# Kernel tuning notes

Hardware: AMD Instinct MI355X
Metric: run time of the kernel (lower is better)

Reference implementation:

```python
import jax, jax.numpy as jnp
import numpy as np
from jax import lax

BN_EPS = 1e-5

def _dw_conv_bn(img, w, g, b, mu, var):
    # img: [B,C,H,W], w: [C,1,3,3] depthwise (feature_group_count=C), stride 1, pad 1
    C = img.shape[1]
    y = lax.conv_general_dilated(img, w, (1, 1), 'SAME',
                                 dimension_numbers=('NCHW', 'OIHW', 'NCHW'),
                                 feature_group_count=C)
    scale = (g / jnp.sqrt(var + BN_EPS))[None, :, None, None]
    return y * scale + (b - mu * g / jnp.sqrt(var + BN_EPS))[None, :, None, None]


def setup_inputs() -> dict:
    key = jax.random.key(0)
    B, H, W, C, Co = 32, 28, 28, 192, 192
    T = 1 + H * W
    ks = jax.random.split(key, 8)
    x = jax.random.normal(ks[0], (B, T, C), dtype=jnp.float32)
    conv_w = jax.random.normal(ks[1], (3, C, 1, 3, 3), dtype=jnp.float32) * 0.1
    bn_scale = 1.0 + 0.1 * jax.random.normal(ks[2], (3, C), dtype=jnp.float32)
    bn_bias = 0.1 * jax.random.normal(ks[3], (3, C), dtype=jnp.float32)
    bn_mean = 0.1 * jax.random.normal(ks[4], (3, C), dtype=jnp.float32)
    bn_var = jax.random.uniform(ks[5], (3, C), dtype=jnp.float32, minval=0.5, maxval=1.5)
    w_qkv = jax.random.normal(ks[6], (3, Co, C), dtype=jnp.float32) / np.sqrt(C)
    kp, kb = jax.random.split(ks[7])
    w_proj = jax.random.normal(kp, (Co, Co), dtype=jnp.float32) / np.sqrt(Co)
    b_proj = 0.01 * jax.random.normal(kb, (Co,), dtype=jnp.float32)
    return {"x": x, "conv_w": conv_w, "bn_scale": bn_scale, "bn_bias": bn_bias,
            "bn_mean": bn_mean, "bn_var": bn_var, "w_qkv": w_qkv,
            "w_proj": w_proj, "b_proj": b_proj, "h": H, "w": W, "num_heads": 3}


def reference(x, conv_w, bn_scale, bn_bias, bn_mean, bn_var, w_qkv, w_proj, b_proj, h, w, num_heads):
    B, T, C = x.shape
    Co = w_proj.shape[0]
    scale = Co ** (-0.5)  # NOTE: module scales by dim_out^-0.5, not per-head
    cls_tok, tok = x[:, :1], x[:, 1:]
    img = tok.reshape(B, h, w, C).transpose(0, 3, 1, 2)  # b (h w) c -> b c h w
    qkv = []
    for i in range(3):  # q, k, v conv projections (depthwise conv + BN inference)
        y = _dw_conv_bn(img, conv_w[i], bn_scale[i], bn_bias[i], bn_mean[i], bn_var[i])
        y = y.reshape(B, C, h * w).transpose(0, 2, 1)  # b c h w -> b (h w) c
        y = jnp.concatenate([cls_tok, y], axis=1)      # prepend cls token
        qkv.append(jnp.einsum('btc,oc->bto', y, w_qkv[i]))
    d = Co // num_heads
    q, k, v = (t.reshape(B, T, num_heads, d).transpose(0, 2, 1, 3) for t in qkv)
    attn = jnp.einsum('bhld,bhtd->bhlt', q, k) * scale
    attn = jax.nn.softmax(attn, axis=-1)
    out = jnp.einsum('bhlt,bhtd->bhld', attn, v)
    out = out.transpose(0, 2, 1, 3).reshape(B, T, Co)
    return out @ w_proj.T + b_proj
```

## Files before the change

kernel.cpp:

```cpp
#include <hip/hip_runtime.h>

#define B_   32
#define Hh   28
#define Ww   28
#define Cc   192
#define T_   785
#define BT_  (B_ * T_)
#define BTC_ ((size_t)BT_ * Cc)
#define SCALE 0.07216878364870323f

typedef __attribute__((ext_vector_type(8))) __bf16 bf16x8;
typedef __attribute__((ext_vector_type(4))) __bf16 bf16x4;
typedef __attribute__((ext_vector_type(4))) float  f32x4;

__device__ __forceinline__ int imin(int a, int b) { return a < b ? a : b; }

__global__ void wcvt_k(const float* __restrict__ src, __bf16* __restrict__ dst, int n) {
  int i = blockIdx.x * 256 + threadIdx.x;
  if (i < n) dst[i] = (__bf16)src[i];
}

__global__ __launch_bounds__(192) void conv3_bn_k(
    const float* __restrict__ x, const float* __restrict__ cw,
    const float* __restrict__ g, const float* __restrict__ bb,
    const float* __restrict__ mu, const float* __restrict__ var,
    __bf16* __restrict__ y)
{
  const int c = threadIdx.x;
  const int h = blockIdx.x;
  const int b = blockIdx.y;
  float w9[3][9], sc[3], sh[3];
#pragma unroll
  for (int br = 0; br < 3; ++br) {
    sc[br] = g[br * Cc + c] * rsqrtf(var[br * Cc + c] + 1e-5f);
    sh[br] = bb[br * Cc + c] - mu[br * Cc + c] * sc[br];
#pragma unroll
    for (int k = 0; k < 9; ++k) w9[br][k] = cw[(br * Cc + c) * 9 + k];
  }
  const float* xb = x + (size_t)b * T_ * Cc;
  if (h == 0) {
#pragma unroll
    for (int br = 0; br < 3; ++br)
      y[br * BTC_ + (size_t)b * T_ * Cc + c] = (__bf16)xb[c];
  }
  float c0[3], c1[3], c2[3];
#pragma unroll
  for (int r = 0; r < 3; ++r) {
    int rr = h - 1 + r;
    c0[r] = 0.f;
    c1[r] = (rr >= 0 && rr < Hh) ? xb[(size_t)(1 + rr * Ww) * Cc + c] : 0.f;
  }
  for (int col = 0; col < Ww; ++col) {
#pragma unroll
    for (int r = 0; r < 3; ++r) {
      int rr = h - 1 + r, ci = col + 1;
      c2[r] = (rr >= 0 && rr < Hh && ci < Ww)
                ? xb[(size_t)(1 + rr * Ww + ci) * Cc + c] : 0.f;
    }
    size_t orow = (size_t)(b * T_ + 1 + h * Ww + col) * Cc + c;
#pragma unroll
    for (int br = 0; br < 3; ++br) {
      float acc = c0[0]*w9[br][0] + c1[0]*w9[br][1] + c2[0]*w9[br][2]
                + c0[1]*w9[br][3] + c1[1]*w9[br][4] + c2[1]*w9[br][5]
                + c0[2]*w9[br][6] + c1[2]*w9[br][7] + c2[2]*w9[br][8];
      y[br * BTC_ + orow] = (__bf16)(acc * sc[br] + sh[br]);
    }
#pragma unroll
    for (int r = 0; r < 3; ++r) { c0[r] = c1[r]; c1[r] = c2[r]; }
  }
}

template <int OUTF32>
__global__ __launch_bounds__(256) void gemm_bf16(
    const __bf16* __restrict__ A, const __bf16* __restrict__ Bw,
    const float* __restrict__ bias, void* __restrict__ outp, float oscale)
{
  __shared__ __bf16 As[128][72];
  __shared__ __bf16 Bs[64][72];
  const int tid = threadIdx.x;
  const int wid = tid >> 6, l = tid & 63, c = l & 15, g = l >> 4;
  const int wm = wid >> 1, wn = wid & 1;
  const int m0 = blockIdx.x * 128, n0 = blockIdx.y * 64;
  const int ar = tid >> 1, ah = tid & 1;
  const int br2 = tid >> 2, bq = tid & 3;

  f32x4 acc[4][2];
#pragma unroll
  for (int i = 0; i < 4; ++i)
#pragma unroll
    for (int j = 0; j < 2; ++j) acc[i][j] = (f32x4)(0.f);

  for (int kc = 0; kc < 3; ++kc) {
    const int k0 = kc * 64;
    const __bf16* ap = A + (size_t)imin(m0 + ar, BT_ - 1) * Cc + k0 + ah * 32;
    const __bf16* bp = Bw + (size_t)(n0 + br2) * Cc + k0 + bq * 16;
    uint4 a0 = *(const uint4*)(ap + 0);
    uint4 a1 = *(const uint4*)(ap + 8);
    uint4 a2 = *(const uint4*)(ap + 16);
    uint4 a3 = *(const uint4*)(ap + 24);
    uint4 b0 = *(const uint4*)(bp + 0);
    uint4 b1 = *(const uint4*)(bp + 8);
    __syncthreads();
    *(uint4*)&As[ar][ah * 32 + 0]  = a0;
    *(uint4*)&As[ar][ah * 32 + 8]  = a1;
    *(uint4*)&As[ar][ah * 32 + 16] = a2;
    *(uint4*)&As[ar][ah * 32 + 24] = a3;
    *(uint4*)&Bs[br2][bq * 16 + 0] = b0;
    *(uint4*)&Bs[br2][bq * 16 + 8] = b1;
    __syncthreads();
#pragma unroll
    for (int ksl = 0; ksl < 2; ++ksl) {
      bf16x8 af[4], bfr[2];
#pragma unroll
      for (int mf = 0; mf < 4; ++mf)
        af[mf] = *(const bf16x8*)&As[wm * 64 + mf * 16 + c][ksl * 32 + g * 8];
#pragma unroll
      for (int nf = 0; nf < 2; ++nf)
        bfr[nf] = *(const bf16x8*)&Bs[wn * 32 + nf * 16 + c][ksl * 32 + g * 8];
#pragma unroll
      for (int mf = 0; mf < 4; ++mf)
#pragma unroll
        for (int nf = 0; nf < 2; ++nf)
          acc[mf][nf] = __builtin_amdgcn_mfma_f32_16x16x32_bf16(
              af[mf], bfr[nf], acc[mf][nf], 0, 0, 0);
    }
  }
  float bias_c[2] = {0.f, 0.f};
  if (OUTF32) {
#pragma unroll
    for (int nf = 0; nf < 2; ++nf) bias_c[nf] = bias[n0 + wn * 32 + nf * 16 + c];
  }
#pragma unroll
  for (int mf = 0; mf < 4; ++mf) {
#pragma unroll
    for (int i = 0; i < 4; ++i) {
      int m = m0 + wm * 64 + mf * 16 + g * 4 + i;
      if (m < BT_) {
#pragma unroll
        for (int nf = 0; nf < 2; ++nf) {
          int n = n0 + wn * 32 + nf * 16 + c;
          if (OUTF32)
            ((float*)outp)[(size_t)m * Cc + n] = acc[mf][nf][i] + bias_c[nf];
          else
            ((__bf16*)outp)[(size_t)m * Cc + n] = (__bf16)(acc[mf][nf][i] * oscale);
        }
      }
    }
  }
}

__global__ __launch_bounds__(256) void attn_mfma(
    const __bf16* __restrict__ qkv, __bf16* __restrict__ aout)
{
  __shared__ __bf16 Ks[64][72];
  __shared__ __bf16 Vt[64][72];
  __shared__ __bf16 Ps[4][16][72];
  const int tid = threadIdx.x;
  const int wid = tid >> 6, l = tid & 63, c = l & 15, g = l >> 4;
  const int qt = blockIdx.x, hh = blockIdx.y, b = blockIdx.z;
  const __bf16* Q = qkv + ((size_t)(0 * B_ + b) * T_) * Cc + hh * 64;
  const __bf16* K = qkv + ((size_t)(1 * B_ + b) * T_) * Cc + hh * 64;
  const __bf16* V = qkv + ((size_t)(2 * B_ + b) * T_) * Cc + hh * 64;

  const int qrow = qt * 64 + wid * 16 + c;
  const __bf16* qp = Q + (size_t)imin(qrow, T_ - 1) * Cc + g * 8;
  bf16x8 qf[2];
  qf[0] = *(const bf16x8*)(qp);
  qf[1] = *(const bf16x8*)(qp + 32);

  const int skey = tid >> 2, sdq = tid & 3;
  const int vkp = tid & 31, vd0 = (tid >> 5) * 8;

  f32x4 ot[4];
#pragma unroll
  for (int f = 0; f < 4; ++f) ot[f] = (f32x4)(0.f);
  float m_run = -1e30f, l_run = 0.f;

  for (int kt = 0; kt < 13; ++kt) {
    __syncthreads();
    {
      const __bf16* kp = K + (size_t)imin(kt * 64 + skey, T_ - 1) * Cc + sdq * 16;
      uint4 k0v = *(const uint4*)(kp + 0);
      uint4 k1v = *(const uint4*)(kp + 8);
      *(uint4*)&Ks[skey][sdq * 16 + 0] = k0v;
      *(uint4*)&Ks[skey][sdq * 16 + 8] = k1v;
      const __bf16* v0 = V + (size_t)imin(kt * 64 + 2 * vkp + 0, T_ - 1) * Cc + vd0;
      const __bf16* v1 = V + (size_t)imin(kt * 64 + 2 * vkp + 1, T_ - 1) * Cc + vd0;
      uint4 va = *(const uint4*)v0;
      uint4 vb = *(const uint4*)v1;
      const ushort* pa = (const ushort*)&va;
      const ushort* pb = (const ushort*)&vb;
#pragma unroll
      for (int e = 0; e < 8; ++e) {
        unsigned pk = (unsigned)pa[e] | ((unsigned)pb[e] << 16);
        *(unsigned*)&Vt[vd0 + e][2 * vkp] = pk;
      }
    }
    __syncthreads();

    f32x4 st[4];
#pragma unroll
    for (int f = 0; f < 4; ++f) st[f] = (f32x4)(0.f);
#pragma unroll
    for (int s = 0; s < 2; ++s) {
#pragma unroll
      for (int f = 0; f < 4; ++f) {
        bf16x8 ka = *(const bf16x8*)&Ks[f * 16 + c][s * 32 + g * 8];
        st[f] = __builtin_amdgcn_mfma_f32_16x16x32_bf16(ka, qf[s], st[f], 0, 0, 0);
      }
    }
    if (kt == 12) {
#pragma unroll
      for (int f = 0; f < 4; ++f)
#pragma unroll
        for (int i = 0; i < 4; ++i)
          if (f * 16 + g * 4 + i >= 17) st[f][i] = -1e30f;
    }
    float pmax = -1e30f;
#pragma unroll
    for (int f = 0; f < 4; ++f)
#pragma unroll
      for (int i = 0; i < 4; ++i) pmax = fmaxf(pmax, st[f][i]);
    pmax = fmaxf(pmax, __shfl_xor(pmax, 16));
    pmax = fmaxf(pmax, __shfl_xor(pmax, 32));
    float mnew = fmaxf(m_run, pmax);
    float corr = __expf(m_run - mnew);
    m_run = mnew;
    float rs = 0.f;
#pragma unroll
    for (int f = 0; f < 4; ++f) {
      bf16x4 pk;
#pragma unroll
      for (int i = 0; i < 4; ++i) {
        float p = __expf(st[f][i] - mnew);
        rs += p;
        pk[i] = (__bf16)p;
      }
      *(bf16x4*)&Ps[wid][c][f * 16 + g * 4] = pk;
    }
    rs += __shfl_xor(rs, 16);
    rs += __shfl_xor(rs, 32);
    l_run = l_run * corr + rs;
#pragma unroll
    for (int f = 0; f < 4; ++f)
#pragma unroll
      for (int i = 0; i < 4; ++i) ot[f][i] *= corr;

#pragma unroll
    for (int s = 0; s < 2; ++s) {
      bf16x8 pb2 = *(const bf16x8*)&Ps[wid][c][s * 32 + g * 8];
#pragma unroll
      for (int f = 0; f < 4; ++f) {
        bf16x8 va2 = *(const bf16x8*)&Vt[f * 16 + c][s * 32 + g * 8];
        ot[f] = __builtin_amdgcn_mfma_f32_16x16x32_bf16(va2, pb2, ot[f], 0, 0, 0);
      }
    }
  }

  const int t = qt * 64 + wid * 16 + c;
  if (t < T_) {
    float inv = l_run > 0.f ? 1.f / l_run : 0.f;
    __bf16* op = aout + ((size_t)(b * T_ + t)) * Cc + hh * 64;
#pragma unroll
    for (int f = 0; f < 4; ++f) {
      bf16x4 ov;
#pragma unroll
      for (int i = 0; i < 4; ++i) ov[i] = (__bf16)(ot[f][i] * inv);
      *(bf16x4*)(op + f * 16 + g * 4) = ov;
    }
  }
}

extern "C" void kernel_launch(void* const* d_in, const int* in_sizes, int n_in,
                              void* d_out, int out_size, void* d_ws, size_t ws_size,
                              hipStream_t stream) {
  (void)in_sizes; (void)n_in; (void)out_size; (void)ws_size;
  const float* x        = (const float*)d_in[0];
  const float* conv_w   = (const float*)d_in[1];
  const float* bn_scale = (const float*)d_in[2];
  const float* bn_bias  = (const float*)d_in[3];
  const float* bn_mean  = (const float*)d_in[4];
  const float* bn_var   = (const float*)d_in[5];
  const float* w_qkv    = (const float*)d_in[6];
  const float* w_proj   = (const float*)d_in[7];
  const float* b_proj   = (const float*)d_in[8];

  __bf16* ybf  = (__bf16*)d_ws;
  __bf16* qkvb = ybf + 3 * BTC_;
  __bf16* aobf = qkvb + 3 * BTC_;
  __bf16* wq   = aobf + BTC_;
  __bf16* wp   = wq + 3 * Cc * Cc;

  wcvt_k<<<(3 * Cc * Cc + 255) / 256, 256, 0, stream>>>(w_qkv, wq, 3 * Cc * Cc);
  wcvt_k<<<(Cc * Cc + 255) / 256, 256, 0, stream>>>(w_proj, wp, Cc * Cc);
  conv3_bn_k<<<dim3(Hh, B_), 192, 0, stream>>>(
      x, conv_w, bn_scale, bn_bias, bn_mean, bn_var, ybf);

  const int mblocks = (BT_ + 127) / 128;
  for (int i = 0; i < 3; ++i) {
    gemm_bf16<0><<<dim3(mblocks, 3), 256, 0, stream>>>(
        ybf + (size_t)i * BTC_, wq + (size_t)i * Cc * Cc, nullptr,
        qkvb + (size_t)i * BTC_, i == 0 ? SCALE : 1.0f);
  }
  attn_mfma<<<dim3(13, 3, B_), 256, 0, stream>>>(qkvb, aobf);
  gemm_bf16<1><<<dim3(mblocks, 3), 256, 0, stream>>>(
      aobf, wp, b_proj, d_out, 1.0f);
}
```

Baseline: 186.7 us.

## Batch launches, prefetch tiles, use exp2 softmax with lazy rescale, swizzle attention blocks

Merges the two weight-conversion launches and the three QKV GEMM launches into single launches, and makes the conv kernel produce two output rows per block to reuse loaded input rows. Both the GEMM and the attention kernel now register-prefetch the next K-chunk or K/V tile while the current one is stored to and computed from shared memory. The attention softmax folds log2(e) into the Q scale so it can use exp2f, and it rescales the running max and accumulator only when the new max exceeds the old one by more than a threshold. Attention blocks are also launched from a 1D swizzled index. These changes aim to cut launch overhead, hide global-load latency and reduce exp and rescale work, at the cost of more registers and a softmax whose unnormalised values may grow before the final divide.

```diff
diff --git a/kernel.cpp b/kernel.cpp
--- a/kernel.cpp
+++ b/kernel.cpp
@@ -7,7 +7,7 @@
 #define T_   785
 #define BT_  (B_ * T_)
 #define BTC_ ((size_t)BT_ * Cc)
-#define SCALE 0.07216878364870323f
+#define SCALE2 0.10412163388f
 
 typedef __attribute__((ext_vector_type(8))) __bf16 bf16x8;
 typedef __attribute__((ext_vector_type(4))) __bf16 bf16x4;
@@ -15,9 +15,11 @@
 
 __device__ __forceinline__ int imin(int a, int b) { return a < b ? a : b; }
 
-__global__ void wcvt_k(const float* __restrict__ src, __bf16* __restrict__ dst, int n) {
+__global__ void wcvt_k(const float* __restrict__ wq, const float* __restrict__ wp,
+                       __bf16* __restrict__ dst) {
   int i = blockIdx.x * 256 + threadIdx.x;
-  if (i < n) dst[i] = (__bf16)src[i];
+  float v = (i < 3 * Cc * Cc) ? wq[i] : wp[i - 3 * Cc * Cc];
+  dst[i] = (__bf16)v;
 }
 
 __global__ __launch_bounds__(192) void conv3_bn_k(
@@ -27,7 +29,7 @@
     __bf16* __restrict__ y)
 {
   const int c = threadIdx.x;
-  const int h = blockIdx.x;
+  const int h0 = blockIdx.x * 2;
   const int b = blockIdx.y;
   float w9[3][9], sc[3], sh[3];
 #pragma unroll
@@ -38,45 +40,52 @@
     for (int k = 0; k < 9; ++k) w9[br][k] = cw[(br * Cc + c) * 9 + k];
   }
   const float* xb = x + (size_t)b * T_ * Cc;
-  if (h == 0) {
+  if (h0 == 0) {
 #pragma unroll
     for (int br = 0; br < 3; ++br)
       y[br * BTC_ + (size_t)b * T_ * Cc + c] = (__bf16)xb[c];
   }
-  float c0[3], c1[3], c2[3];
-#pragma unroll
-  for (int r = 0; r < 3; ++r) {
-    int rr = h - 1 + r;
+  float c0[4], c1[4], c2[4];
+#pragma unroll
+  for (int r = 0; r < 4; ++r) {
+    int rr = h0 - 1 + r;
     c0[r] = 0.f;
     c1[r] = (rr >= 0 && rr < Hh) ? xb[(size_t)(1 + rr * Ww) * Cc + c] : 0.f;
   }
   for (int col = 0; col < Ww; ++col) {
 #pragma unroll
-    for (int r = 0; r < 3; ++r) {
-      int rr = h - 1 + r, ci = col + 1;
+    for (int r = 0; r < 4; ++r) {
+      int rr = h0 - 1 + r, ci = col + 1;
       c2[r] = (rr >= 0 && rr < Hh && ci < Ww)
                 ? xb[(size_t)(1 + rr * Ww + ci) * Cc + c] : 0.f;
     }
-    size_t orow = (size_t)(b * T_ + 1 + h * Ww + col) * Cc + c;
-#pragma unroll
-    for (int br = 0; br < 3; ++br) {
-      float acc = c0[0]*w9[br][0] + c1[0]*w9[br][1] + c2[0]*w9[br][2]
-                + c0[1]*w9[br][3] + c1[1]*w9[br][4] + c2[1]*w9[br][5]
-                + c0[2]*w9[br][6] + c1[2]*w9[br][7] + c2[2]*w9[br][8];
-      y[br * BTC_ + orow] = (__bf16)(acc * sc[br] + sh[br]);
-    }
-#pragma unroll
-    for (int r = 0; r < 3; ++r) { c0[r] = c1[r]; c1[r] = c2[r]; }
-  }
-}
-
-template <int OUTF32>
+#pragma unroll
+    for (int ro = 0; ro < 2; ++ro) {
+      size_t orow = (size_t)(b * T_ + 1 + (h0 + ro) * Ww + col) * Cc + c;
+#pragma unroll
+      for (int br = 0; br < 3; ++br) {
+        float acc = c0[ro+0]*w9[br][0] + c1[ro+0]*w9[br][1] + c2[ro+0]*w9[br][2]
+                  + c0[ro+1]*w9[br][3] + c1[ro+1]*w9[br][4] + c2[ro+1]*w9[br][5]
+                  + c0[ro+2]*w9[br][6] + c1[ro+2]*w9[br][7] + c2[ro+2]*w9[br][8];
+        y[br * BTC_ + orow] = (__bf16)(acc * sc[br] + sh[br]);
+      }
+    }
+#pragma unroll
+    for (int r = 0; r < 4; ++r) { c0[r] = c1[r]; c1[r] = c2[r]; }
+  }
+}
+
+template <int MODE>
 __global__ __launch_bounds__(256) void gemm_bf16(
-    const __bf16* __restrict__ A, const __bf16* __restrict__ Bw,
-    const float* __restrict__ bias, void* __restrict__ outp, float oscale)
+    const __bf16* __restrict__ A0, const __bf16* __restrict__ W0,
+    const float* __restrict__ bias, void* __restrict__ outp)
 {
   __shared__ __bf16 As[128][72];
   __shared__ __bf16 Bs[64][72];
+  const int z = blockIdx.z;
+  const __bf16* A  = A0 + (MODE == 0 ? (size_t)z * BTC_ : 0);
+  const __bf16* Bw = W0 + (MODE == 0 ? (size_t)z * Cc * Cc : 0);
+  const float oscale = (MODE == 0 && z == 0) ? SCALE2 : 1.0f;
   const int tid = threadIdx.x;
   const int wid = tid >> 6, l = tid & 63, c = l & 15, g = l >> 4;
   const int wm = wid >> 1, wn = wid & 1;
@@ -90,16 +99,16 @@
 #pragma unroll
     for (int j = 0; j < 2; ++j) acc[i][j] = (f32x4)(0.f);
 
+  const __bf16* ap = A + (size_t)imin(m0 + ar, BT_ - 1) * Cc + ah * 32;
+  const __bf16* bp = Bw + (size_t)(n0 + br2) * Cc + bq * 16;
+  uint4 a0 = *(const uint4*)(ap + 0);
+  uint4 a1 = *(const uint4*)(ap + 8);
+  uint4 a2 = *(const uint4*)(ap + 16);
+  uint4 a3 = *(const uint4*)(ap + 24);
+  uint4 b0 = *(const uint4*)(bp + 0);
+  uint4 b1 = *(const uint4*)(bp + 8);
+
   for (int kc = 0; kc < 3; ++kc) {
-    const int k0 = kc * 64;
-    const __bf16* ap = A + (size_t)imin(m0 + ar, BT_ - 1) * Cc + k0 + ah * 32;
-    const __bf16* bp = Bw + (size_t)(n0 + br2) * Cc + k0 + bq * 16;
-    uint4 a0 = *(const uint4*)(ap + 0);
-    uint4 a1 = *(const uint4*)(ap + 8);
-    uint4 a2 = *(const uint4*)(ap + 16);
-    uint4 a3 = *(const uint4*)(ap + 24);
-    uint4 b0 = *(const uint4*)(bp + 0);
-    uint4 b1 = *(const uint4*)(bp + 8);
     __syncthreads();
     *(uint4*)&As[ar][ah * 32 + 0]  = a0;
     *(uint4*)&As[ar][ah * 32 + 8]  = a1;
@@ -107,6 +116,15 @@
     *(uint4*)&As[ar][ah * 32 + 24] = a3;
     *(uint4*)&Bs[br2][bq * 16 + 0] = b0;
     *(uint4*)&Bs[br2][bq * 16 + 8] = b1;
+    if (kc < 2) {
+      ap += 64; bp += 64;
+      a0 = *(const uint4*)(ap + 0);
+      a1 = *(const uint4*)(ap + 8);
+      a2 = *(const uint4*)(ap + 16);
+      a3 = *(const uint4*)(ap + 24);
+      b0 = *(const uint4*)(bp + 0);
+      b1 = *(const uint4*)(bp + 8);
+    }
     __syncthreads();
 #pragma unroll
     for (int ksl = 0; ksl < 2; ++ksl) {
@@ -126,7 +144,7 @@
     }
   }
   float bias_c[2] = {0.f, 0.f};
-  if (OUTF32) {
+  if (MODE == 1) {
 #pragma unroll
     for (int nf = 0; nf < 2; ++nf) bias_c[nf] = bias[n0 + wn * 32 + nf * 16 + c];
   }
@@ -139,10 +157,11 @@
 #pragma unroll
         for (int nf = 0; nf < 2; ++nf) {
           int n = n0 + wn * 32 + nf * 16 + c;
-          if (OUTF32)
+          if (MODE == 1)
             ((float*)outp)[(size_t)m * Cc + n] = acc[mf][nf][i] + bias_c[nf];
           else
-            ((__bf16*)outp)[(size_t)m * Cc + n] = (__bf16)(acc[mf][nf][i] * oscale);
+            ((__bf16*)outp)[z * BTC_ + (size_t)m * Cc + n] =
+                (__bf16)(acc[mf][nf][i] * oscale);
         }
       }
     }
@@ -155,9 +174,14 @@
   __shared__ __bf16 Ks[64][72];
   __shared__ __bf16 Vt[64][72];
   __shared__ __bf16 Ps[4][16][72];
+  const int bid = blockIdx.x;
+  const int swz = (bid & 7) * 156 + (bid >> 3);
+  const int qt = swz % 13;
+  const int g2 = swz / 13;
+  const int hh = g2 % 3;
+  const int b  = g2 / 3;
   const int tid = threadIdx.x;
   const int wid = tid >> 6, l = tid & 63, c = l & 15, g = l >> 4;
-  const int qt = blockIdx.x, hh = blockIdx.y, b = blockIdx.z;
   const __bf16* Q = qkv + ((size_t)(0 * B_ + b) * T_) * Cc + hh * 64;
   const __bf16* K = qkv + ((size_t)(1 * B_ + b) * T_) * Cc + hh * 64;
   const __bf16* V = qkv + ((size_t)(2 * B_ + b) * T_) * Cc + hh * 64;
@@ -171,6 +195,18 @@
   const int skey = tid >> 2, sdq = tid & 3;
   const int vkp = tid & 31, vd0 = (tid >> 5) * 8;
 
+  uint4 kr0, kr1, va, vb;
+  auto loadKV = [&](int kt2) {
+    const __bf16* kp = K + (size_t)imin(kt2 * 64 + skey, T_ - 1) * Cc + sdq * 16;
+    kr0 = *(const uint4*)(kp + 0);
+    kr1 = *(const uint4*)(kp + 8);
+    const __bf16* v0 = V + (size_t)imin(kt2 * 64 + 2 * vkp + 0, T_ - 1) * Cc + vd0;
+    const __bf16* v1 = V + (size_t)imin(kt2 * 64 + 2 * vkp + 1, T_ - 1) * Cc + vd0;
+    va = *(const uint4*)v0;
+    vb = *(const uint4*)v1;
+  };
+  loadKV(0);
+
   f32x4 ot[4];
 #pragma unroll
   for (int f = 0; f < 4; ++f) ot[f] = (f32x4)(0.f);
@@ -178,24 +214,18 @@
 
   for (int kt = 0; kt < 13; ++kt) {
     __syncthreads();
+    *(uint4*)&Ks[skey][sdq * 16 + 0] = kr0;
+    *(uint4*)&Ks[skey][sdq * 16 + 8] = kr1;
     {
-      const __bf16* kp = K + (size_t)imin(kt * 64 + skey, T_ - 1) * Cc + sdq * 16;
-      uint4 k0v = *(const uint4*)(kp + 0);
-      uint4 k1v = *(const uint4*)(kp + 8);
-      *(uint4*)&Ks[skey][sdq * 16 + 0] = k0v;
-      *(uint4*)&Ks[skey][sdq * 16 + 8] = k1v;
-      const __bf16* v0 = V + (size_t)imin(kt * 64 + 2 * vkp + 0, T_ - 1) * Cc + vd0;
-      const __bf16* v1 = V + (size_t)imin(kt * 64 + 2 * vkp + 1, T_ - 1) * Cc + vd0;
-      uint4 va = *(const uint4*)v0;
-      uint4 vb = *(const uint4*)v1;
       const ushort* pa = (const ushort*)&va;
       const ushort* pb = (const ushort*)&vb;
 #pragma unroll
       for (int e = 0; e < 8; ++e) {
-        unsigned pk = (unsigned)pa[e] | ((unsigned)pb[e] << 16);
-        *(unsigned*)&Vt[vd0 + e][2 * vkp] = pk;
-      }
-    }
+        unsigned pk2 = (unsigned)pa[e] | ((unsigned)pb[e] << 16);
+        *(unsigned*)&Vt[vd0 + e][2 * vkp] = pk2;
+      }
+    }
+    if (kt < 12) loadKV(kt + 1);
     __syncthreads();
 
     f32x4 st[4];
@@ -223,16 +253,23 @@
       for (int i = 0; i < 4; ++i) pmax = fmaxf(pmax, st[f][i]);
     pmax = fmaxf(pmax, __shfl_xor(pmax, 16));
     pmax = fmaxf(pmax, __shfl_xor(pmax, 32));
-    float mnew = fmaxf(m_run, pmax);
-    float corr = __expf(m_run - mnew);
-    m_run = mnew;
+    if (!__all(pmax <= m_run + 8.f)) {
+      float mnew = fmaxf(m_run, pmax);
+      float corr = exp2f(m_run - mnew);
+      m_run = mnew;
+      l_run *= corr;
+#pragma unroll
+      for (int f = 0; f < 4; ++f)
+#pragma unroll
+        for (int i = 0; i < 4; ++i) ot[f][i] *= corr;
+    }
     float rs = 0.f;
 #pragma unroll
     for (int f = 0; f < 4; ++f) {
       bf16x4 pk;
 #pragma unroll
       for (int i = 0; i < 4; ++i) {
-        float p = __expf(st[f][i] - mnew);
+        float p = exp2f(st[f][i] - m_run);
         rs += p;
         pk[i] = (__bf16)p;
       }
@@ -240,11 +277,7 @@
     }
     rs += __shfl_xor(rs, 16);
     rs += __shfl_xor(rs, 32);
-    l_run = l_run * corr + rs;
-#pragma unroll
-    for (int f = 0; f < 4; ++f)
-#pragma unroll
-      for (int i = 0; i < 4; ++i) ot[f][i] *= corr;
+    l_run += rs;
 
 #pragma unroll
     for (int s = 0; s < 2; ++s) {
@@ -259,7 +292,7 @@
 
   const int t = qt * 64 + wid * 16 + c;
   if (t < T_) {
-    float inv = l_run > 0.f ? 1.f / l_run : 0.f;
+    float inv = 1.f / l_run;
     __bf16* op = aout + ((size_t)(b * T_ + t)) * Cc + hh * 64;
 #pragma unroll
     for (int f = 0; f < 4; ++f) {
@@ -291,18 +324,12 @@
   __bf16* wq   = aobf + BTC_;
   __bf16* wp   = wq + 3 * Cc * Cc;
 
-  wcvt_k<<<(3 * Cc * Cc + 255) / 256, 256, 0, stream>>>(w_qkv, wq, 3 * Cc * Cc);
-  wcvt_k<<<(Cc * Cc + 255) / 256, 256, 0, stream>>>(w_proj, wp, Cc * Cc);
-  conv3_bn_k<<<dim3(Hh, B_), 192, 0, stream>>>(
+  wcvt_k<<<576, 256, 0, stream>>>(w_qkv, w_proj, wq);
+  conv3_bn_k<<<dim3(14, B_), 192, 0, stream>>>(
       x, conv_w, bn_scale, bn_bias, bn_mean, bn_var, ybf);
 
   const int mblocks = (BT_ + 127) / 128;
-  for (int i = 0; i < 3; ++i) {
-    gemm_bf16<0><<<dim3(mblocks, 3), 256, 0, stream>>>(
-        ybf + (size_t)i * BTC_, wq + (size_t)i * Cc * Cc, nullptr,
-        qkvb + (size_t)i * BTC_, i == 0 ? SCALE : 1.0f);
-  }
-  attn_mfma<<<dim3(13, 3, B_), 256, 0, stream>>>(qkvb, aobf);
-  gemm_bf16<1><<<dim3(mblocks, 3), 256, 0, stream>>>(
-      aobf, wp, b_proj, d_out, 1.0f);
-}
+  gemm_bf16<0><<<dim3(mblocks, 3, 3), 256, 0, stream>>>(ybf, wq, nullptr, qkvb);
+  attn_mfma<<<1248, 256, 0, stream>>>(qkvb, aobf);
+  gemm_bf16<1><<<dim3(mblocks, 3, 1), 256, 0, stream>>>(aobf, wp, b_proj, d_out);
+}
```

New measurement: 181.7 us. 1.03x faster.
